# Kernel optimization log

Hardware: AMD Instinct MI355X
Metric: run time of the kernel (lower is better)

The kernel has to match this reference:

```python
import jax, jax.numpy as jnp
import numpy as np

D_MODEL = 768
NUM_HEADS = 12
HEAD_DIM = D_MODEL // NUM_HEADS
BATCH = 1
SEQ = 4096


def setup_inputs() -> dict:
    key = jax.random.key(0)
    ks = jax.random.split(key, 11)
    s = 0.02
    return {
        "q": jax.random.normal(ks[0], (BATCH, SEQ, D_MODEL), jnp.float32),
        "k": jax.random.normal(ks[1], (BATCH, SEQ, D_MODEL), jnp.float32),
        "v": jax.random.normal(ks[2], (BATCH, SEQ, D_MODEL), jnp.float32),
        "Wq": jax.random.normal(ks[3], (D_MODEL, D_MODEL), jnp.float32) * s,
        "bq": jnp.zeros((D_MODEL,), jnp.float32),
        "Wk": jax.random.normal(ks[4], (D_MODEL, D_MODEL), jnp.float32) * s,
        "bk": jnp.zeros((D_MODEL,), jnp.float32),
        "Wv": jax.random.normal(ks[5], (D_MODEL, D_MODEL), jnp.float32) * s,
        "bv": jnp.zeros((D_MODEL,), jnp.float32),
        "Wo": jax.random.normal(ks[6], (D_MODEL, D_MODEL), jnp.float32) * s,
        "bo": jnp.zeros((D_MODEL,), jnp.float32),
    }


def reference(q, k, v, Wq, bq, Wk, bk, Wv, bv, Wo, bo):
    B, S, D = q.shape
    H, Hd = NUM_HEADS, HEAD_DIM
    # linear projections (torch Linear: x @ W.T + b)
    qh = (q @ Wq.T + bq).reshape(B, S, H, Hd).transpose(0, 2, 1, 3)  # [B,H,S,Hd]
    kh = (k @ Wk.T + bk).reshape(B, S, H, Hd).transpose(0, 2, 1, 3)
    vh = (v @ Wv.T + bv).reshape(B, S, H, Hd).transpose(0, 2, 1, 3)
    scale = 1.0 / jnp.sqrt(jnp.asarray(Hd, qh.dtype))
    scores = jnp.einsum("bhsd,bhtd->bhst", qh, kh) * scale  # [B,H,S,S]
    weights = jax.nn.softmax(scores, axis=-1)
    attn = jnp.einsum("bhst,bhtd->bhsd", weights, vh)  # [B,H,S,Hd]
    attn = attn.transpose(0, 2, 1, 3).reshape(B, S, D)
    return attn @ Wo.T + bo
```

## Files before the change

### kernel.cpp

```cpp
#include <hip/hip_runtime.h>

#define S_LEN 4096
#define DMODEL 768
#define NHEAD 12
#define HD 64

typedef __bf16 bf16x8 __attribute__((ext_vector_type(8)));
typedef __bf16 bf16x4 __attribute__((ext_vector_type(4)));
typedef float f32x4 __attribute__((ext_vector_type(4)));
typedef float f32x16 __attribute__((ext_vector_type(16)));
typedef unsigned short u16x8 __attribute__((ext_vector_type(8)));
typedef unsigned short u16x4 __attribute__((ext_vector_type(4)));
typedef _Float16 f16x4 __attribute__((ext_vector_type(4)));

#if __has_builtin(__builtin_amdgcn_exp2f)
#define EXP2F(x) __builtin_amdgcn_exp2f(x)
#else
#define EXP2F(x) exp2f(x)
#endif

#define MFMA32(a, b, c) __builtin_amdgcn_mfma_f32_32x32x16_bf16(a, b, c, 0, 0, 0)

__device__ __forceinline__ unsigned short f2bf(float f) {
  unsigned int u = __float_as_uint(f);
  u += 0x7fffu + ((u >> 16) & 1u);
  return (unsigned short)(u >> 16);
}

__device__ __forceinline__ void gload_lds16(const void* g, void* l) {
  __builtin_amdgcn_global_load_lds(
      (__attribute__((address_space(1))) void*)g,
      (__attribute__((address_space(3))) void*)l, 16, 0, 0);
}

struct CvtArgs {
  const float* src[7];
  unsigned short* dst[7];
  int n[7];
};

__global__ __launch_bounds__(256) void cvt_kernel(CvtArgs a) {
  const int seg = blockIdx.y;
  const int n = a.n[seg];
  const int i = (blockIdx.x * 256 + threadIdx.x) * 8;
  if (i >= n) return;
  const float* s = a.src[seg] + i;
  u16x8 o;
#pragma unroll
  for (int j = 0; j < 8; ++j) o[j] = f2bf(s[j]);
  *reinterpret_cast<u16x8*>(a.dst[seg] + i) = o;
}

struct QkvArgs {
  const unsigned short* A[3];
  const unsigned short* W[3];
  const float* bias[3];
  unsigned short* dst[3];
  float scale[3];
};

__global__ __launch_bounds__(256) void qkv_gemm(QkvArgs a) {
  __shared__ unsigned char lds[32768];
  const int z = blockIdx.z;
  const unsigned short* __restrict__ A = a.A[z];
  const unsigned short* __restrict__ B = a.W[z];
  const float* __restrict__ bias = a.bias[z];
  unsigned short* __restrict__ dst = a.dst[z];
  const float scale = a.scale[z];

  const int tid = threadIdx.x;
  const int lane = tid & 63;
  const int w = tid >> 6;
  const int wr = w >> 1, wc = w & 1;
  const int c = lane & 15, g = lane >> 4;
  const int m0 = blockIdx.x * 128;
  const int n0 = blockIdx.y * 128;

  f32x4 acc[4][4] = {};

  for (int kt = 0; kt < DMODEL / 64; ++kt) {
#pragma unroll
    for (int p = 0; p < 4; ++p) {
      const int te = p * 256 + tid;
      const int row = te >> 3;
      const int sb = ((te & 7) * 16) ^ ((row & 7) << 4);
      gload_lds16(A + (size_t)(m0 + row) * DMODEL + kt * 64 + (sb >> 1), &lds[te * 16]);
      gload_lds16(B + (size_t)(n0 + row) * DMODEL + kt * 64 + (sb >> 1), &lds[16384 + te * 16]);
    }
    __syncthreads();

    bf16x8 af[4][2], bfr[4][2];
#pragma unroll
    for (int mb = 0; mb < 4; ++mb)
#pragma unroll
      for (int ks = 0; ks < 2; ++ks) {
        const int row = wr * 64 + mb * 16 + c;
        const int byte = (ks * 64 + g * 16) ^ ((row & 7) << 4);
        af[mb][ks] = *reinterpret_cast<const bf16x8*>(&lds[row * 128 + byte]);
      }
#pragma unroll
    for (int nb = 0; nb < 4; ++nb)
#pragma unroll
      for (int ks = 0; ks < 2; ++ks) {
        const int row = wc * 64 + nb * 16 + c;
        const int byte = (ks * 64 + g * 16) ^ ((row & 7) << 4);
        bfr[nb][ks] = *reinterpret_cast<const bf16x8*>(&lds[16384 + row * 128 + byte]);
      }
    __builtin_amdgcn_s_setprio(1);
#pragma unroll
    for (int ks = 0; ks < 2; ++ks)
#pragma unroll
      for (int mb = 0; mb < 4; ++mb)
#pragma unroll
        for (int nb = 0; nb < 4; ++nb)
          acc[mb][nb] = __builtin_amdgcn_mfma_f32_16x16x32_bf16(
              af[mb][ks], bfr[nb][ks], acc[mb][nb], 0, 0, 0);
    __builtin_amdgcn_s_setprio(0);
    __syncthreads();
  }

#pragma unroll
  for (int mb = 0; mb < 4; ++mb) {
#pragma unroll
    for (int nb = 0; nb < 4; ++nb) {
      const int n = n0 + wc * 64 + nb * 16 + c;
      const float bv = bias[n];
#pragma unroll
      for (int r = 0; r < 4; ++r) {
        const int m = m0 + wr * 64 + mb * 16 + g * 4 + r;
        const float v = (acc[mb][nb][r] + bv) * scale;
        const int hh = n >> 6, hd = n & 63;
        if (z != 2) {
          dst[((size_t)hh * S_LEN + m) * HD + hd] = f2bf(v);
        } else {
          const int mp = (m & ~12) | ((m & 4) << 1) | ((m & 8) >> 1);
          dst[((size_t)hh * HD + hd) * S_LEN + mp] = f2bf(v);
        }
      }
    }
  }
}

__global__ __launch_bounds__(256) void gemm_out(
    const unsigned short* __restrict__ A, const unsigned short* __restrict__ B,
    const float* __restrict__ bias, float* __restrict__ dst) {
  __shared__ unsigned char lds[32768];
  const int tid = threadIdx.x;
  const int lane = tid & 63;
  const int w = tid >> 6;
  const int wr = w >> 1, wc = w & 1;
  const int c = lane & 15, g = lane >> 4;
  const int m0 = blockIdx.x * 128;
  const int n0 = blockIdx.y * 128;

  f32x4 acc[4][4] = {};

  for (int kt = 0; kt < DMODEL / 64; ++kt) {
#pragma unroll
    for (int p = 0; p < 4; ++p) {
      const int te = p * 256 + tid;
      const int row = te >> 3;
      const int sb = ((te & 7) * 16) ^ ((row & 7) << 4);
      gload_lds16(A + (size_t)(m0 + row) * DMODEL + kt * 64 + (sb >> 1), &lds[te * 16]);
      gload_lds16(B + (size_t)(n0 + row) * DMODEL + kt * 64 + (sb >> 1), &lds[16384 + te * 16]);
    }
    __syncthreads();

    bf16x8 af[4][2], bfr[4][2];
#pragma unroll
    for (int mb = 0; mb < 4; ++mb)
#pragma unroll
      for (int ks = 0; ks < 2; ++ks) {
        const int row = wr * 64 + mb * 16 + c;
        const int byte = (ks * 64 + g * 16) ^ ((row & 7) << 4);
        af[mb][ks] = *reinterpret_cast<const bf16x8*>(&lds[row * 128 + byte]);
      }
#pragma unroll
    for (int nb = 0; nb < 4; ++nb)
#pragma unroll
      for (int ks = 0; ks < 2; ++ks) {
        const int row = wc * 64 + nb * 16 + c;
        const int byte = (ks * 64 + g * 16) ^ ((row & 7) << 4);
        bfr[nb][ks] = *reinterpret_cast<const bf16x8*>(&lds[16384 + row * 128 + byte]);
      }
    __builtin_amdgcn_s_setprio(1);
#pragma unroll
    for (int ks = 0; ks < 2; ++ks)
#pragma unroll
      for (int mb = 0; mb < 4; ++mb)
#pragma unroll
        for (int nb = 0; nb < 4; ++nb)
          acc[mb][nb] = __builtin_amdgcn_mfma_f32_16x16x32_bf16(
              af[mb][ks], bfr[nb][ks], acc[mb][nb], 0, 0, 0);
    __builtin_amdgcn_s_setprio(0);
    __syncthreads();
  }

#pragma unroll
  for (int mb = 0; mb < 4; ++mb)
#pragma unroll
    for (int nb = 0; nb < 4; ++nb) {
      const int n = n0 + wc * 64 + nb * 16 + c;
      const float bv = bias[n];
#pragma unroll
      for (int r = 0; r < 4; ++r) {
        const int m = m0 + wr * 64 + mb * 16 + g * 4 + r;
        dst[(size_t)m * DMODEL + n] = acc[mb][nb][r] + bv;
      }
    }
}

__global__ __launch_bounds__(512, 4) void attn_kernel(
    const unsigned short* __restrict__ qh,
    const unsigned short* __restrict__ kh,
    const unsigned short* __restrict__ vtp,
    _Float16* __restrict__ pacc,
    float* __restrict__ prs) {
  __shared__ unsigned char lds[49152];
  const int tid = threadIdx.x;
  const int lane = tid & 63;
  const int w = tid >> 6;
  const int c5 = lane & 31;
  const int h2 = lane >> 5;
  const int hh = blockIdx.y;
  const int split = blockIdx.z;
  const int qw = blockIdx.x * 256 + w * 32;
  const int kv0 = split * (S_LEN / 4);
  const int nkt = (S_LEN / 4) / 64;

  bf16x8 qa[4];
#pragma unroll
  for (int ks = 0; ks < 4; ++ks)
    qa[ks] = *reinterpret_cast<const bf16x8*>(
        qh + ((size_t)hh * S_LEN + qw + c5) * HD + ks * 16 + h2 * 8);

  const unsigned short* ksrc =
      kh + ((size_t)hh * S_LEN + kv0 + (tid & 63)) * HD + (tid >> 6) * 8;
  const unsigned short* vsrc =
      vtp + ((size_t)hh * HD + (tid & 63)) * S_LEN + kv0 + (tid >> 6) * 8;
  const int dL = tid * 16;

  auto stage = [&](int bo) {
    gload_lds16(ksrc, &lds[bo + dL]);
    gload_lds16(vsrc, &lds[bo + 8192 + dL]);
    ksrc += 64 * HD;
    vsrc += 64;
  };

  stage(0);
  stage(16384);

  f32x16 accO[2] = {};
  float rs0 = 0.f, rs1 = 0.f, rs2 = 0.f, rs3 = 0.f;

  auto compute = [&](const unsigned char* Kb, const unsigned char* Vb) {
    f32x16 s0 = {}, s1 = {};
    __builtin_amdgcn_s_setprio(1);
#pragma unroll
    for (int ks = 0; ks < 4; ++ks) {
      const unsigned char* kbase = Kb + (ks * 2 + h2) * 1024 + c5 * 16;
      const bf16x8 k0 = *reinterpret_cast<const bf16x8*>(kbase);
      const bf16x8 k1 = *reinterpret_cast<const bf16x8*>(kbase + 512);
      s0 = MFMA32(k0, qa[ks], s0);
      s1 = MFMA32(k1, qa[ks], s1);
    }
    __builtin_amdgcn_s_setprio(0);

#pragma unroll
    for (int t = 0; t < 2; ++t)
#pragma unroll
      for (int ss = 0; ss < 2; ++ss) {
        const unsigned char* vbase = Vb + (t * 4 + ss * 2 + h2) * 1024 + c5 * 16;
        const bf16x8 va0 = *reinterpret_cast<const bf16x8*>(vbase);
        const bf16x8 va1 = *reinterpret_cast<const bf16x8*>(vbase + 512);
        bf16x8 pb;
        float racc = 0.f;
#pragma unroll
        for (int r = 0; r < 8; ++r) {
          const float e = EXP2F(t ? s1[ss * 8 + r] : s0[ss * 8 + r]);
          racc += e;
          pb[r] = (__bf16)e;
        }
        if (t == 0) { if (ss == 0) rs0 += racc; else rs1 += racc; }
        else        { if (ss == 0) rs2 += racc; else rs3 += racc; }
        __builtin_amdgcn_s_setprio(1);
        accO[0] = MFMA32(va0, pb, accO[0]);
        accO[1] = MFMA32(va1, pb, accO[1]);
        __builtin_amdgcn_s_setprio(0);
      }
  };

  int boC = 0;
  int boS = 32768;
  for (int t = 0; t < nkt; ++t) {
    if (t + 2 < nkt) {
      asm volatile("s_waitcnt vmcnt(2)" ::: "memory");
      __builtin_amdgcn_sched_barrier(0);
      __builtin_amdgcn_s_barrier();
      __builtin_amdgcn_sched_barrier(0);
      stage(boS);
    } else if (t + 1 < nkt) {
      asm volatile("s_waitcnt vmcnt(2)" ::: "memory");
      __builtin_amdgcn_sched_barrier(0);
      __builtin_amdgcn_s_barrier();
      __builtin_amdgcn_sched_barrier(0);
    } else {
      asm volatile("s_waitcnt vmcnt(0)" ::: "memory");
      __builtin_amdgcn_sched_barrier(0);
      __builtin_amdgcn_s_barrier();
      __builtin_amdgcn_sched_barrier(0);
    }
    compute(&lds[boC], &lds[boC + 8192]);
    boC += 16384; if (boC == 49152) boC = 0;
    boS += 16384; if (boS == 49152) boS = 0;
  }

  float rsA = (rs0 + rs1) + (rs2 + rs3);
  rsA += __shfl_xor(rsA, 32);
  const size_t hqbase = ((size_t)split * NHEAD + hh) * S_LEN + qw + c5;
  if (h2 == 0) prs[hqbase] = rsA * 0.015625f;
#pragma unroll
  for (int dt = 0; dt < 2; ++dt)
#pragma unroll
    for (int rr = 0; rr < 4; ++rr) {
      f16x4 o;
#pragma unroll
      for (int j = 0; j < 4; ++j)
        o[j] = (_Float16)(accO[dt][rr * 4 + j] * 0.015625f);
      *reinterpret_cast<f16x4*>(
          pacc + hqbase * 64 + dt * 32 + rr * 8 + h2 * 4) = o;
    }
}

__global__ __launch_bounds__(256) void combine_kernel(
    const _Float16* __restrict__ pacc, const float* __restrict__ prs,
    unsigned short* __restrict__ attb) {
  const int idx = blockIdx.x * 256 + threadIdx.x;
  const int hq = idx >> 4;
  const int d4 = (idx & 15) * 4;
  const int h = hq >> 12;
  const int q = hq & 4095;
  const int HS = NHEAD * S_LEN;
  const size_t o0 = (size_t)hq * 64 + d4;
  float acc4[4] = {0.f, 0.f, 0.f, 0.f};
  float rs = 0.f;
#pragma unroll
  for (int k = 0; k < 4; ++k) {
    const f16x4 av = *reinterpret_cast<const f16x4*>(pacc + o0 + (size_t)k * HS * 64);
#pragma unroll
    for (int j = 0; j < 4; ++j) acc4[j] += (float)av[j];
    rs += prs[hq + k * HS];
  }
  const float inv = 1.f / rs;
  u16x4 ov;
#pragma unroll
  for (int j = 0; j < 4; ++j) ov[j] = f2bf(acc4[j] * inv);
  *reinterpret_cast<u16x4*>(attb + (size_t)q * DMODEL + h * HD + d4) = ov;
}

extern "C" void kernel_launch(void* const* d_in, const int* in_sizes, int n_in,
                              void* d_out, int out_size, void* d_ws, size_t ws_size,
                              hipStream_t stream) {
  (void)in_sizes; (void)n_in; (void)out_size;
  const float* q  = (const float*)d_in[0];
  const float* k  = (const float*)d_in[1];
  const float* v  = (const float*)d_in[2];
  const float* Wq = (const float*)d_in[3];
  const float* bq = (const float*)d_in[4];
  const float* Wk = (const float*)d_in[5];
  const float* bk = (const float*)d_in[6];
  const float* Wv = (const float*)d_in[7];
  const float* bv = (const float*)d_in[8];
  const float* Wo = (const float*)d_in[9];
  const float* bo = (const float*)d_in[10];
  float* out = (float*)d_out;

  const size_t SD = (size_t)S_LEN * DMODEL;
  const size_t DD = (size_t)DMODEL * DMODEL;
  if (ws_size < (7 * SD + 4 * DD) * 2) return;

  unsigned short* ws   = (unsigned short*)d_ws;
  unsigned short* qbf  = ws;
  unsigned short* kbf  = ws + SD;
  unsigned short* vbf  = ws + 2 * SD;
  unsigned short* wqb  = ws + 3 * SD;
  unsigned short* wkb  = ws + 3 * SD + DD;
  unsigned short* wvb  = ws + 3 * SD + 2 * DD;
  unsigned short* qhb  = ws + 4 * SD;
  unsigned short* khb  = ws + 5 * SD;
  unsigned short* vtb  = ws + 6 * SD;
  float*          prs  = (float*)(ws + 7 * SD);
  unsigned short* wob  = ws + 7 * SD + 393216;
  _Float16*       pacc = (_Float16*)ws;
  unsigned short* attb = ws + 4 * SD;

  CvtArgs ca;
  ca.src[0] = q;  ca.dst[0] = qbf; ca.n[0] = (int)SD;
  ca.src[1] = k;  ca.dst[1] = kbf; ca.n[1] = (int)SD;
  ca.src[2] = v;  ca.dst[2] = vbf; ca.n[2] = (int)SD;
  ca.src[3] = Wq; ca.dst[3] = wqb; ca.n[3] = (int)DD;
  ca.src[4] = Wk; ca.dst[4] = wkb; ca.n[4] = (int)DD;
  ca.src[5] = Wv; ca.dst[5] = wvb; ca.n[5] = (int)DD;
  ca.src[6] = Wo; ca.dst[6] = wob; ca.n[6] = (int)DD;
  cvt_kernel<<<dim3(1536, 7), 256, 0, stream>>>(ca);

  QkvArgs qa;
  qa.A[0] = qbf; qa.W[0] = wqb; qa.bias[0] = bq; qa.dst[0] = qhb;
  qa.scale[0] = 0.18033688011112042f;
  qa.A[1] = kbf; qa.W[1] = wkb; qa.bias[1] = bk; qa.dst[1] = khb;
  qa.scale[1] = 1.0f;
  qa.A[2] = vbf; qa.W[2] = wvb; qa.bias[2] = bv; qa.dst[2] = vtb;
  qa.scale[2] = 1.0f;
  qkv_gemm<<<dim3(32, 6, 3), 256, 0, stream>>>(qa);

  attn_kernel<<<dim3(S_LEN / 256, NHEAD, 4), 512, 0, stream>>>(
      qhb, khb, vtb, pacc, prs);

  combine_kernel<<<dim3((NHEAD * S_LEN * 16) / 256), 256, 0, stream>>>(
      pacc, prs, attb);

  gemm_out<<<dim3(32, 6), 256, 0, stream>>>(attb, wob, bo, out);
}
```

Baseline: 121.6 us.

## Fuse fp32-to-bf16 conversion into QKV GEMM and split-combine into output GEMM

The QKV projection GEMM now reads the fp32 activations directly and converts them to bf16 while staging into LDS, so the separate conversion pass over q/k/v and its workspace round-trip are gone. The output GEMM now reads the four fp16 split partial accumulators and row sums itself, reduces and normalizes them with a reciprocal, and writes bf16 into LDS, which removes the combine kernel and its intermediate buffer. The A-operand loads become synchronous register loads instead of direct global-to-LDS copies. The split reduction is recomputed by each of the six column-tile blocks, and the partials are now summed in fp16 before the multiply.

```diff
diff --git a/kernel.cpp b/kernel.cpp
--- a/kernel.cpp
+++ b/kernel.cpp
@@ -12,6 +12,7 @@
 typedef unsigned short u16x8 __attribute__((ext_vector_type(8)));
 typedef unsigned short u16x4 __attribute__((ext_vector_type(4)));
 typedef _Float16 f16x4 __attribute__((ext_vector_type(4)));
+typedef _Float16 f16x8 __attribute__((ext_vector_type(8)));
 
 #if __has_builtin(__builtin_amdgcn_exp2f)
 #define EXP2F(x) __builtin_amdgcn_exp2f(x)
@@ -19,6 +20,12 @@
 #define EXP2F(x) exp2f(x)
 #endif
 
+#if __has_builtin(__builtin_amdgcn_rcpf)
+#define RCPF(x) __builtin_amdgcn_rcpf(x)
+#else
+#define RCPF(x) (1.0f / (x))
+#endif
+
 #define MFMA32(a, b, c) __builtin_amdgcn_mfma_f32_32x32x16_bf16(a, b, c, 0, 0, 0)
 
 __device__ __forceinline__ unsigned short f2bf(float f) {
@@ -34,16 +41,13 @@
 }
 
 struct CvtArgs {
-  const float* src[7];
-  unsigned short* dst[7];
-  int n[7];
+  const float* src[4];
+  unsigned short* dst[4];
 };
 
 __global__ __launch_bounds__(256) void cvt_kernel(CvtArgs a) {
   const int seg = blockIdx.y;
-  const int n = a.n[seg];
   const int i = (blockIdx.x * 256 + threadIdx.x) * 8;
-  if (i >= n) return;
   const float* s = a.src[seg] + i;
   u16x8 o;
 #pragma unroll
@@ -52,7 +56,7 @@
 }
 
 struct QkvArgs {
-  const unsigned short* A[3];
+  const float* A[3];
   const unsigned short* W[3];
   const float* bias[3];
   unsigned short* dst[3];
@@ -62,7 +66,7 @@
 __global__ __launch_bounds__(256) void qkv_gemm(QkvArgs a) {
   __shared__ unsigned char lds[32768];
   const int z = blockIdx.z;
-  const unsigned short* __restrict__ A = a.A[z];
+  const float* __restrict__ A = a.A[z];
   const unsigned short* __restrict__ B = a.W[z];
   const float* __restrict__ bias = a.bias[z];
   unsigned short* __restrict__ dst = a.dst[z];
@@ -84,8 +88,21 @@
       const int te = p * 256 + tid;
       const int row = te >> 3;
       const int sb = ((te & 7) * 16) ^ ((row & 7) << 4);
-      gload_lds16(A + (size_t)(m0 + row) * DMODEL + kt * 64 + (sb >> 1), &lds[te * 16]);
-      gload_lds16(B + (size_t)(n0 + row) * DMODEL + kt * 64 + (sb >> 1), &lds[16384 + te * 16]);
+      const float* src = A + (size_t)(m0 + row) * DMODEL + kt * 64 + (sb >> 1);
+      const f32x4 lo = *reinterpret_cast<const f32x4*>(src);
+      const f32x4 hi = *reinterpret_cast<const f32x4*>(src + 4);
+      bf16x8 v;
+#pragma unroll
+      for (int j = 0; j < 4; ++j) { v[j] = (__bf16)lo[j]; v[4 + j] = (__bf16)hi[j]; }
+      *reinterpret_cast<bf16x8*>(&lds[te * 16]) = v;
+    }
+#pragma unroll
+    for (int p = 0; p < 4; ++p) {
+      const int te = p * 256 + tid;
+      const int row = te >> 3;
+      const int sb = ((te & 7) * 16) ^ ((row & 7) << 4);
+      gload_lds16(B + (size_t)(n0 + row) * DMODEL + kt * 64 + (sb >> 1),
+                  &lds[16384 + te * 16]);
     }
     __syncthreads();
 
@@ -142,8 +159,10 @@
 }
 
 __global__ __launch_bounds__(256) void gemm_out(
-    const unsigned short* __restrict__ A, const unsigned short* __restrict__ B,
-    const float* __restrict__ bias, float* __restrict__ dst) {
+    const _Float16* __restrict__ pacc,
+    const float* __restrict__ prs,
+    const unsigned short* __restrict__ B, const float* __restrict__ bias,
+    float* __restrict__ dst) {
   __shared__ unsigned char lds[32768];
   const int tid = threadIdx.x;
   const int lane = tid & 63;
@@ -152,6 +171,8 @@
   const int c = lane & 15, g = lane >> 4;
   const int m0 = blockIdx.x * 128;
   const int n0 = blockIdx.y * 128;
+  const int HS = NHEAD * S_LEN;
+  const int HS64 = HS * 64;
 
   f32x4 acc[4][4] = {};
 
@@ -161,8 +182,29 @@
       const int te = p * 256 + tid;
       const int row = te >> 3;
       const int sb = ((te & 7) * 16) ^ ((row & 7) << 4);
-      gload_lds16(A + (size_t)(m0 + row) * DMODEL + kt * 64 + (sb >> 1), &lds[te * 16]);
-      gload_lds16(B + (size_t)(n0 + row) * DMODEL + kt * 64 + (sb >> 1), &lds[16384 + te * 16]);
+      const int s = m0 + row;
+      const size_t base = ((size_t)kt * S_LEN + s) * 64 + (sb >> 1);
+      const f16x8 a0 = *reinterpret_cast<const f16x8*>(pacc + base);
+      const f16x8 a1 = *reinterpret_cast<const f16x8*>(pacc + base + HS64);
+      const f16x8 a2 = *reinterpret_cast<const f16x8*>(pacc + base + 2 * (size_t)HS64);
+      const f16x8 a3 = *reinterpret_cast<const f16x8*>(pacc + base + 3 * (size_t)HS64);
+      const int pidx = kt * S_LEN + s;
+      const float rsum = (prs[pidx] + prs[pidx + HS]) +
+                         (prs[pidx + 2 * HS] + prs[pidx + 3 * HS]);
+      const float inv = RCPF(rsum);
+      const f16x8 sum = (a0 + a1) + (a2 + a3);
+      bf16x8 v;
+#pragma unroll
+      for (int j = 0; j < 8; ++j) v[j] = (__bf16)((float)sum[j] * inv);
+      *reinterpret_cast<bf16x8*>(&lds[te * 16]) = v;
+    }
+#pragma unroll
+    for (int p = 0; p < 4; ++p) {
+      const int te = p * 256 + tid;
+      const int row = te >> 3;
+      const int sb = ((te & 7) * 16) ^ ((row & 7) << 4);
+      gload_lds16(B + (size_t)(n0 + row) * DMODEL + kt * 64 + (sb >> 1),
+                  &lds[16384 + te * 16]);
     }
     __syncthreads();
 
@@ -332,32 +374,6 @@
     }
 }
 
-__global__ __launch_bounds__(256) void combine_kernel(
-    const _Float16* __restrict__ pacc, const float* __restrict__ prs,
-    unsigned short* __restrict__ attb) {
-  const int idx = blockIdx.x * 256 + threadIdx.x;
-  const int hq = idx >> 4;
-  const int d4 = (idx & 15) * 4;
-  const int h = hq >> 12;
-  const int q = hq & 4095;
-  const int HS = NHEAD * S_LEN;
-  const size_t o0 = (size_t)hq * 64 + d4;
-  float acc4[4] = {0.f, 0.f, 0.f, 0.f};
-  float rs = 0.f;
-#pragma unroll
-  for (int k = 0; k < 4; ++k) {
-    const f16x4 av = *reinterpret_cast<const f16x4*>(pacc + o0 + (size_t)k * HS * 64);
-#pragma unroll
-    for (int j = 0; j < 4; ++j) acc4[j] += (float)av[j];
-    rs += prs[hq + k * HS];
-  }
-  const float inv = 1.f / rs;
-  u16x4 ov;
-#pragma unroll
-  for (int j = 0; j < 4; ++j) ov[j] = f2bf(acc4[j] * inv);
-  *reinterpret_cast<u16x4*>(attb + (size_t)q * DMODEL + h * HD + d4) = ov;
-}
-
 extern "C" void kernel_launch(void* const* d_in, const int* in_sizes, int n_in,
                               void* d_out, int out_size, void* d_ws, size_t ws_size,
                               hipStream_t stream) {
@@ -380,44 +396,34 @@
   if (ws_size < (7 * SD + 4 * DD) * 2) return;
 
   unsigned short* ws   = (unsigned short*)d_ws;
-  unsigned short* qbf  = ws;
-  unsigned short* kbf  = ws + SD;
-  unsigned short* vbf  = ws + 2 * SD;
-  unsigned short* wqb  = ws + 3 * SD;
-  unsigned short* wkb  = ws + 3 * SD + DD;
-  unsigned short* wvb  = ws + 3 * SD + 2 * DD;
+  unsigned short* wqb  = ws;
+  unsigned short* wkb  = ws + DD;
+  unsigned short* wvb  = ws + 2 * DD;
   unsigned short* qhb  = ws + 4 * SD;
   unsigned short* khb  = ws + 5 * SD;
   unsigned short* vtb  = ws + 6 * SD;
   float*          prs  = (float*)(ws + 7 * SD);
   unsigned short* wob  = ws + 7 * SD + 393216;
   _Float16*       pacc = (_Float16*)ws;
-  unsigned short* attb = ws + 4 * SD;
 
   CvtArgs ca;
-  ca.src[0] = q;  ca.dst[0] = qbf; ca.n[0] = (int)SD;
-  ca.src[1] = k;  ca.dst[1] = kbf; ca.n[1] = (int)SD;
-  ca.src[2] = v;  ca.dst[2] = vbf; ca.n[2] = (int)SD;
-  ca.src[3] = Wq; ca.dst[3] = wqb; ca.n[3] = (int)DD;
-  ca.src[4] = Wk; ca.dst[4] = wkb; ca.n[4] = (int)DD;
-  ca.src[5] = Wv; ca.dst[5] = wvb; ca.n[5] = (int)DD;
-  ca.src[6] = Wo; ca.dst[6] = wob; ca.n[6] = (int)DD;
-  cvt_kernel<<<dim3(1536, 7), 256, 0, stream>>>(ca);
+  ca.src[0] = Wq; ca.dst[0] = wqb;
+  ca.src[1] = Wk; ca.dst[1] = wkb;
+  ca.src[2] = Wv; ca.dst[2] = wvb;
+  ca.src[3] = Wo; ca.dst[3] = wob;
+  cvt_kernel<<<dim3(288, 4), 256, 0, stream>>>(ca);
 
   QkvArgs qa;
-  qa.A[0] = qbf; qa.W[0] = wqb; qa.bias[0] = bq; qa.dst[0] = qhb;
+  qa.A[0] = q; qa.W[0] = wqb; qa.bias[0] = bq; qa.dst[0] = qhb;
   qa.scale[0] = 0.18033688011112042f;
-  qa.A[1] = kbf; qa.W[1] = wkb; qa.bias[1] = bk; qa.dst[1] = khb;
+  qa.A[1] = k; qa.W[1] = wkb; qa.bias[1] = bk; qa.dst[1] = khb;
   qa.scale[1] = 1.0f;
-  qa.A[2] = vbf; qa.W[2] = wvb; qa.bias[2] = bv; qa.dst[2] = vtb;
+  qa.A[2] = v; qa.W[2] = wvb; qa.bias[2] = bv; qa.dst[2] = vtb;
   qa.scale[2] = 1.0f;
   qkv_gemm<<<dim3(32, 6, 3), 256, 0, stream>>>(qa);
 
   attn_kernel<<<dim3(S_LEN / 256, NHEAD, 4), 512, 0, stream>>>(
       qhb, khb, vtb, pacc, prs);
 
-  combine_kernel<<<dim3((NHEAD * S_LEN * 16) / 256), 256, 0, stream>>>(
-      pacc, prs, attb);
-
-  gemm_out<<<dim3(32, 6), 256, 0, stream>>>(attb, wob, bo, out);
-}
+  gemm_out<<<dim3(32, 6), 256, 0, stream>>>(pacc, prs, wob, bo, out);
+}
```

New measurement: 125.8 us. +3.5%, slower.
